# Optimization experiments

Measured on AMD Instinct MI355X. Metric: run time of the kernel, lower is better.

## Reference

```python
import jax, jax.numpy as jnp
from jax import lax
import numpy as np

# Finite stand-in for torch's -inf mask value; avoids inf/nan issues under AD
# while leaving the argmax-based selection identical (kernel entries are O(1)).
NEG_MASK = -1e30


def cdpruner_select(image_features, last_layer_attention_avg_image, topk):
    """Greedy DPP (fast-MAP) token selection; faithful port of cdpruner().
    image_features: (B, N, D); last_layer_attention_avg_image: (B, N).
    Returns selected indices for batch 0, shape (topk,).
    """
    B, N, D = image_features.shape
    xn = image_features / jnp.linalg.norm(image_features, axis=-1, keepdims=True)
    xn = xn.astype(jnp.float32)
    similarity = jnp.einsum('bnd,bmd->bnm', xn, xn)          # (B, N, N)
    rel = -last_layer_attention_avg_image.astype(jnp.float32)
    rel = (rel - rel.min() + 1e-6) / (rel.max() - rel.min())  # global min/max, like torch .min()/.max()
    kernel = rel[:, :, None] * similarity * rel[:, None, :]   # (B, N, N)

    di2s0 = jnp.diagonal(kernel, axis1=1, axis2=2)            # (B, N)
    cis0 = jnp.zeros((topk, B, N), jnp.float32)
    bar = jnp.arange(B)

    def step(carry, i):
        cis, di2s = carry
        j = jnp.argmax(di2s, axis=-1)                         # (B,)
        kj = kernel[bar, j]                                   # (B, N)
        cis_j = cis[:, bar, j]                                # (topk, B); rows >= i are zero
        proj = jnp.einsum('tb,tbn->bn', cis_j, cis)           # == sum over first i rows
        eis = (kj - proj) / jnp.sqrt(di2s[bar, j])[:, None]   # (B, N)
        cis = cis.at[i].set(eis)
        di2s = di2s - jnp.square(eis)
        di2s = di2s.at[bar, j].set(NEG_MASK)
        return (cis, di2s), j

    _, js = lax.scan(step, (cis0, di2s0), jnp.arange(topk))   # js: (topk, B)
    return js[:, 0]                                           # select_idx.t()[0]


def setup_inputs() -> dict:
    key = jax.random.key(0)
    k1, k2 = jax.random.split(key)
    B, N, D = 1, 4096, 1024
    return {
        'image_features': jax.random.normal(k1, (B, N, D), jnp.float32),
        'last_layer_attention_avg_image': jax.random.uniform(k2, (B, N), jnp.float32),
        'topk_image_token_num': 128,
    }


def reference(image_features, last_layer_attention_avg_image, topk_image_token_num):
    sel = cdpruner_select(image_features, last_layer_attention_avg_image,
                          topk_image_token_num)
    # Downstream the model gathers the kept tokens; return the pruned features
    # (float output, shape (topk, D)) so fwd and fwd+bwd references agree.
    return image_features[0, sel]
```

## Files before the change

kernel.cpp:

```cpp
#include <hip/hip_runtime.h>
#include <hip/hip_bf16.h>
#include <stdint.h>

#define NTOK 4096
#define DIM  1024
#define TOPK 128
#define GB   32
#define GT   128
#define NEGM -1e30f

typedef __attribute__((ext_vector_type(8))) short bf16x8;
typedef __attribute__((ext_vector_type(4))) float f32x4;

__global__ __launch_bounds__(1024) void k_prep(const float* __restrict__ attn,
                                               float* __restrict__ rel) {
  __shared__ float smx[16], smn[16];
  int tid = threadIdx.x;
  float mx = -3.4e38f, mn = 3.4e38f;
  for (int n = tid; n < NTOK; n += 1024) {
    float a = attn[n];
    mx = fmaxf(mx, a); mn = fminf(mn, a);
  }
  for (int o = 32; o >= 1; o >>= 1) {
    mx = fmaxf(mx, __shfl_down(mx, o, 64));
    mn = fminf(mn, __shfl_down(mn, o, 64));
  }
  if ((tid & 63) == 0) { smx[tid >> 6] = mx; smn[tid >> 6] = mn; }
  __syncthreads();
  if (tid == 0) {
    float MX = smx[0], MN = smn[0];
    for (int w = 1; w < 16; ++w) { MX = fmaxf(MX, smx[w]); MN = fminf(MN, smn[w]); }
    smx[0] = MX; smn[0] = MN;
  }
  __syncthreads();
  float amax = smx[0], amin = smn[0];
  float rmin  = -amax;
  float range = (-amin) - rmin;
  for (int n = tid; n < NTOK; n += 1024) {
    float r = -attn[n];
    rel[n] = ((r - rmin) + 1e-6f) / range;
  }
}

__global__ __launch_bounds__(256) void k_norm(const float* __restrict__ x,
                                              __hip_bfloat16* __restrict__ H,
                                              __hip_bfloat16* __restrict__ L) {
  __shared__ float ps[4];
  int row = blockIdx.x, tid = threadIdx.x;
  const float4* xr = (const float4*)(x + (size_t)row * DIM);
  float4 v = xr[tid];
  float s = v.x * v.x + v.y * v.y + v.z * v.z + v.w * v.w;
  for (int o = 32; o >= 1; o >>= 1) s += __shfl_down(s, o, 64);
  if ((tid & 63) == 0) ps[tid >> 6] = s;
  __syncthreads();
  if (tid == 0) ps[0] = ps[0] + ps[1] + ps[2] + ps[3];
  __syncthreads();
  float nrm = sqrtf(ps[0]);
  float xf[4] = {v.x / nrm, v.y / nrm, v.z / nrm, v.w / nrm};
  __hip_bfloat16 hh[4], ll[4];
#pragma unroll
  for (int e = 0; e < 4; ++e) {
    hh[e] = __float2bfloat16(xf[e]);
    float lof = xf[e] - __bfloat162float(hh[e]);
    ll[e] = __float2bfloat16(lof);
  }
  *(short4*)(H + (size_t)row * DIM + tid * 4) = *(short4*)hh;
  *(short4*)(L + (size_t)row * DIM + tid * 4) = *(short4*)ll;
}

#define GBK 64
__global__ __launch_bounds__(256) void k_gemm(const __hip_bfloat16* __restrict__ H,
                                              const __hip_bfloat16* __restrict__ L,
                                              const float* __restrict__ rel,
                                              float* __restrict__ ker) {
  int bi = blockIdx.y, bj = blockIdx.x;
  if (bi > bj) return;
  __shared__ __align__(16) char smem[36864];
  int tid = threadIdx.x;
  int lane = tid & 63, wid = tid >> 6;
  int wr = wid >> 1, wc = wid & 1;
  int lm = lane & 15, quad = lane >> 4;
  const __hip_bfloat16* PA[4] = {H, H, L, L};
  const __hip_bfloat16* PB[4] = {H, L, H, L};
  int lr = tid >> 1;
  int lg = (tid & 1) * 32;
  f32x4 acc[4][4];
#pragma unroll
  for (int r = 0; r < 4; ++r)
#pragma unroll
    for (int c = 0; c < 4; ++c) acc[r][c] = (f32x4){0.f, 0.f, 0.f, 0.f};
  bf16x8 pa[4], pb[4];
  {
    const __hip_bfloat16* ag = PA[0] + (size_t)(bi * 128 + lr) * DIM + lg;
    const __hip_bfloat16* bg = PB[0] + (size_t)(bj * 128 + lr) * DIM + lg;
#pragma unroll
    for (int j = 0; j < 4; ++j) {
      pa[j] = *(const bf16x8*)(ag + j * 8);
      pb[j] = *(const bf16x8*)(bg + j * 8);
    }
  }
  for (int kt = 0; kt < 4096; kt += GBK) {
    __syncthreads();
#pragma unroll
    for (int j = 0; j < 4; ++j) {
      *(bf16x8*)(smem + lr * 144 + lg * 2 + j * 16) = pa[j];
      *(bf16x8*)(smem + 18432 + lr * 144 + lg * 2 + j * 16) = pb[j];
    }
    __syncthreads();
    int kn = kt + GBK;
    if (kn < 4096) {
      int p = kn >> 10, kk = kn & 1023;
      const __hip_bfloat16* ag = PA[p] + (size_t)(bi * 128 + lr) * DIM + kk + lg;
      const __hip_bfloat16* bg = PB[p] + (size_t)(bj * 128 + lr) * DIM + kk + lg;
#pragma unroll
      for (int j = 0; j < 4; ++j) {
        pa[j] = *(const bf16x8*)(ag + j * 8);
        pb[j] = *(const bf16x8*)(bg + j * 8);
      }
    }
#pragma unroll
    for (int kq = 0; kq < GBK; kq += 32) {
      bf16x8 af[4], bff[4];
#pragma unroll
      for (int r = 0; r < 4; ++r)
        af[r] = *(const bf16x8*)(smem + (wr * 64 + r * 16 + lm) * 144 +
                                 (kq + quad * 8) * 2);
#pragma unroll
      for (int c = 0; c < 4; ++c)
        bff[c] = *(const bf16x8*)(smem + 18432 + (wc * 64 + c * 16 + lm) * 144 +
                                  (kq + quad * 8) * 2);
#pragma unroll
      for (int r = 0; r < 4; ++r)
#pragma unroll
        for (int c = 0; c < 4; ++c)
          acc[r][c] = __builtin_amdgcn_mfma_f32_16x16x32_bf16(
              af[r], bff[c], acc[r][c], 0, 0, 0);
    }
  }
  float rr[16], rc[4];
#pragma unroll
  for (int r = 0; r < 4; ++r)
#pragma unroll
    for (int e = 0; e < 4; ++e)
      rr[r * 4 + e] = rel[bi * 128 + wr * 64 + r * 16 + quad * 4 + e];
#pragma unroll
  for (int c = 0; c < 4; ++c) rc[c] = rel[bj * 128 + wc * 64 + c * 16 + lm];
#pragma unroll
  for (int r = 0; r < 4; ++r) {
    int grow = bi * 128 + wr * 64 + r * 16 + quad * 4;
#pragma unroll
    for (int c = 0; c < 4; ++c) {
      int gcol = bj * 128 + wc * 64 + c * 16 + lm;
#pragma unroll
      for (int e = 0; e < 4; ++e)
        ker[(size_t)(grow + e) * NTOK + gcol] =
            (acc[r][c][e] * rr[r * 4 + e]) * rc[c];
    }
  }
  if (bi != bj) {
    __syncthreads();
    float* Tw = (float*)(smem + wid * 4672);
#pragma unroll
    for (int c = 0; c < 4; ++c) {
#pragma unroll
      for (int r = 0; r < 4; ++r)
#pragma unroll
        for (int e = 0; e < 4; ++e)
          Tw[lm * 73 + r * 16 + quad * 4 + e] =
              (acc[r][c][e] * rc[c]) * rr[r * 4 + e];
      __syncthreads();
      int cc2 = lane >> 2, seg = lane & 3;
      float* dst = &ker[(size_t)(bj * 128 + wc * 64 + c * 16 + cc2) * NTOK +
                        bi * 128 + wr * 64 + seg * 16];
#pragma unroll
      for (int e = 0; e < 4; ++e)
        *(float4*)&dst[e * 4] = *(const float4*)&Tw[cc2 * 73 + seg * 16 + e * 4];
      __syncthreads();
    }
  }
}

__global__ __launch_bounds__(GT) void k_greedy(const float* __restrict__ ker,
                                               const float* __restrict__ feat,
                                               float* __restrict__ out,
                                               float* __restrict__ cisT,
                                               unsigned long long* __restrict__ slots) {
  __shared__ __align__(16) float histT[GT][132];
  __shared__ __align__(16) float colbuf[TOPK];
  __shared__ unsigned long long redw[GT / 64];
  __shared__ unsigned long long bwS;
  __shared__ int selj[TOPK];
  int tid = threadIdx.x;
  int lane = tid & 63, wid = tid >> 6;
  int blk = blockIdx.x;
  int n = blk * GT + tid;
  float di2s = ker[(size_t)n * NTOK + n];
#pragma unroll
  for (int t = 0; t < TOPK; t += 4)
    *(float4*)&histT[tid][t] = (float4){0.f, 0.f, 0.f, 0.f};

  for (int i = 0; i < TOPK; ++i) {
    unsigned u = __float_as_uint(di2s);
    unsigned key = (u & 0x80000000u) ? ~u : (u | 0x80000000u);
    unsigned long long pk =
        ((unsigned long long)key << 32) | (unsigned)(NTOK - 1 - n);
    for (int o = 32; o >= 1; o >>= 1) {
      unsigned long long q = __shfl_down(pk, o, 64);
      if (q > pk) pk = q;
    }
    if (lane == 0) redw[wid] = pk;
    __syncthreads();
    if (tid == 0) {
      unsigned long long m = redw[0];
      if (redw[1] > m) m = redw[1];
      __hip_atomic_store(&slots[((size_t)i * GB + blk) * 8], m,
                         __ATOMIC_RELEASE, __HIP_MEMORY_SCOPE_AGENT);
    }
    if (wid == 0) {
      unsigned long long v = 0;
      if (lane < GB) {
        do {
          v = __hip_atomic_load(&slots[((size_t)i * GB + lane) * 8],
                                __ATOMIC_RELAXED, __HIP_MEMORY_SCOPE_AGENT);
        } while (v == 0);
      }
      unsigned long long b1 = v;
      for (int o = 32; o >= 1; o >>= 1) {
        unsigned long long q = __shfl_down(b1, o, 64);
        if (q > b1) b1 = q;
      }
      b1 = __shfl(b1, 0, 64);
      __builtin_amdgcn_fence(__ATOMIC_ACQUIRE, "agent");
      int jw = NTOK - 1 - (int)(b1 & 0xffffffffu);
      unsigned long long cu = __hip_atomic_load(
          (const unsigned long long*)(cisT + (size_t)jw * TOPK) + lane,
          __ATOMIC_RELAXED, __HIP_MEMORY_SCOPE_AGENT);
      union { unsigned long long u64; float f[2]; } cc; cc.u64 = cu;
      colbuf[lane * 2]     = cc.f[0];
      colbuf[lane * 2 + 1] = cc.f[1];
      if (lane == 0) bwS = b1;
    }
    __syncthreads();
    unsigned long long b1 = bwS;
    int j = NTOK - 1 - (int)(b1 & 0xffffffffu);
    unsigned kw = (unsigned)(b1 >> 32);
    unsigned du = (kw & 0x80000000u) ? (kw & 0x7fffffffu) : ~kw;
    float sd = sqrtf(__uint_as_float(du));
    if (tid == 0) selj[i] = j;
    float kj = ker[(size_t)j * NTOK + n];
    float proj = 0.f;
    for (int t = 0; t < i; t += 4) {
      float4 c4 = *(const float4*)&colbuf[t];
      float4 h4 = *(const float4*)&histT[tid][t];
      proj += c4.x * h4.x + c4.y * h4.y + c4.z * h4.z + c4.w * h4.w;
    }
    float eis = (kj - proj) / sd;
    __hip_atomic_store(&cisT[(size_t)n * TOPK + i], eis, __ATOMIC_RELAXED,
                       __HIP_MEMORY_SCOPE_AGENT);
    histT[tid][i] = eis;
    di2s -= eis * eis;
    if (n == j) di2s = NEGM;
  }
  __syncthreads();
  for (int k = blk; k < TOPK; k += GB) {
    int j = selj[k];
    const float4* src = (const float4*)(feat + (size_t)j * DIM);
    float4* dst = (float4*)(out + (size_t)k * DIM);
    dst[tid]       = src[tid];
    dst[tid + GT]  = src[tid + GT];
  }
}

extern "C" void kernel_launch(void* const* d_in, const int* in_sizes, int n_in,
                              void* d_out, int out_size, void* d_ws, size_t ws_size,
                              hipStream_t stream) {
  const float* feat = (const float*)d_in[0];
  const float* attn = (const float*)d_in[1];
  float* out = (float*)d_out;
  char* ws = (char*)d_ws;

  unsigned long long* slots = (unsigned long long*)ws;
  float* rel = (float*)(ws + 262144);
  __hip_bfloat16* H = (__hip_bfloat16*)(ws + (1 << 20));
  __hip_bfloat16* L = (__hip_bfloat16*)(ws + (1 << 20) + (8 << 20));
  float* cisT = (float*)(ws + (1 << 20) + (16 << 20));
  float* ker  = (float*)(ws + (1 << 20) + (16 << 20) + (4 << 20));

  hipMemsetAsync(d_ws, 0, 262144, stream);
  k_prep<<<1, 1024, 0, stream>>>(attn, rel);
  k_norm<<<NTOK, 256, 0, stream>>>(feat, H, L);
  k_gemm<<<dim3(32, 32), 256, 0, stream>>>(H, L, rel, ker);
  k_greedy<<<GB, GT, 0, stream>>>(ker, feat, out, cisT, slots);
}
```

Baseline: 656.4 us.

## Load GEMM tiles directly into LDS via global_load_lds with XOR swizzle

```diff
diff --git a/kernel.cpp b/kernel.cpp
--- a/kernel.cpp
+++ b/kernel.cpp
@@ -82,53 +82,49 @@
   int lm = lane & 15, quad = lane >> 4;
   const __hip_bfloat16* PA[4] = {H, H, L, L};
   const __hip_bfloat16* PB[4] = {H, L, H, L};
-  int lr = tid >> 1;
-  int lg = (tid & 1) * 32;
+  int srow = wid * 32 + (lane >> 3);
+  int kcs  = (lane & 7) ^ ((lane >> 3) & 7);
   f32x4 acc[4][4];
 #pragma unroll
   for (int r = 0; r < 4; ++r)
 #pragma unroll
     for (int c = 0; c < 4; ++c) acc[r][c] = (f32x4){0.f, 0.f, 0.f, 0.f};
-  bf16x8 pa[4], pb[4];
-  {
-    const __hip_bfloat16* ag = PA[0] + (size_t)(bi * 128 + lr) * DIM + lg;
-    const __hip_bfloat16* bg = PB[0] + (size_t)(bj * 128 + lr) * DIM + lg;
-#pragma unroll
-    for (int j = 0; j < 4; ++j) {
-      pa[j] = *(const bf16x8*)(ag + j * 8);
-      pb[j] = *(const bf16x8*)(bg + j * 8);
-    }
-  }
+
   for (int kt = 0; kt < 4096; kt += GBK) {
-    __syncthreads();
-#pragma unroll
-    for (int j = 0; j < 4; ++j) {
-      *(bf16x8*)(smem + lr * 144 + lg * 2 + j * 16) = pa[j];
-      *(bf16x8*)(smem + 18432 + lr * 144 + lg * 2 + j * 16) = pb[j];
-    }
-    __syncthreads();
-    int kn = kt + GBK;
-    if (kn < 4096) {
-      int p = kn >> 10, kk = kn & 1023;
-      const __hip_bfloat16* ag = PA[p] + (size_t)(bi * 128 + lr) * DIM + kk + lg;
-      const __hip_bfloat16* bg = PB[p] + (size_t)(bj * 128 + lr) * DIM + kk + lg;
-#pragma unroll
-      for (int j = 0; j < 4; ++j) {
-        pa[j] = *(const bf16x8*)(ag + j * 8);
-        pb[j] = *(const bf16x8*)(bg + j * 8);
-      }
-    }
-#pragma unroll
-    for (int kq = 0; kq < GBK; kq += 32) {
+    int p = kt >> 10, kk = kt & 1023;
+    const __hip_bfloat16* Ab = PA[p] + (size_t)(bi * 128) * DIM + kk;
+    const __hip_bfloat16* Bb = PB[p] + (size_t)(bj * 128) * DIM + kk;
+    __syncthreads();
+#pragma unroll
+    for (int q = 0; q < 4; ++q) {
+      const __hip_bfloat16* ga = Ab + (size_t)(srow + q * 8) * DIM + kcs * 8;
+      const __hip_bfloat16* gb = Bb + (size_t)(srow + q * 8) * DIM + kcs * 8;
+      __builtin_amdgcn_global_load_lds(
+          (const __attribute__((address_space(1))) void*)ga,
+          (__attribute__((address_space(3))) void*)(smem + (wid * 4 + q) * 1024),
+          16, 0, 0);
+      __builtin_amdgcn_global_load_lds(
+          (const __attribute__((address_space(1))) void*)gb,
+          (__attribute__((address_space(3))) void*)(smem + 16384 +
+                                                    (wid * 4 + q) * 1024),
+          16, 0, 0);
+    }
+    __syncthreads();
+#pragma unroll
+    for (int kq = 0; kq < 2; ++kq) {
+      int kc = kq * 4 + quad;
       bf16x8 af[4], bff[4];
 #pragma unroll
-      for (int r = 0; r < 4; ++r)
-        af[r] = *(const bf16x8*)(smem + (wr * 64 + r * 16 + lm) * 144 +
-                                 (kq + quad * 8) * 2);
-#pragma unroll
-      for (int c = 0; c < 4; ++c)
-        bff[c] = *(const bf16x8*)(smem + 18432 + (wc * 64 + c * 16 + lm) * 144 +
-                                  (kq + quad * 8) * 2);
+      for (int r = 0; r < 4; ++r) {
+        int row = wr * 64 + r * 16 + lm;
+        af[r] = *(const bf16x8*)(smem + row * 128 + ((kc ^ (lm & 7)) * 16));
+      }
+#pragma unroll
+      for (int c = 0; c < 4; ++c) {
+        int row = wc * 64 + c * 16 + lm;
+        bff[c] = *(const bf16x8*)(smem + 16384 + row * 128 +
+                                  ((kc ^ (lm & 7)) * 16));
+      }
 #pragma unroll
       for (int r = 0; r < 4; ++r)
 #pragma unroll
```

New measurement: 638.2 us. -2.8%, faster.
